# Performance work log

Measured on AMD Instinct MI355X. Metric: run time of the kernel, lower is better.

## Reference

```python
import jax, jax.numpy as jnp
import numpy as np

EPS = 1e-7
BETA = 1.0


def setup_inputs() -> dict:
    key = jax.random.key(0)
    k1, k2, k3, k4 = jax.random.split(key, 4)
    N, E, D_IN, D_OUT = 50000, 800000, 96, 96
    feat = jax.random.normal(k1, (N, D_IN), dtype=jnp.float32)
    src = jax.random.randint(k2, (E,), 0, N, dtype=jnp.int32)
    dst = jax.random.randint(k3, (E,), 0, N, dtype=jnp.int32)
    W = jax.random.normal(k4, (D_IN, D_OUT), dtype=jnp.float32) / np.sqrt(D_IN)
    b = jnp.zeros((D_OUT,), dtype=jnp.float32)
    return {"feat": feat, "src": src, "dst": dst, "W": W, "b": b}


def reference(feat, src, dst, W, b):
    # GENConv with softmax aggregation (canonical DeeperGCN semantics):
    # per edge e=(u,v): m_e = relu(h_u) + eps
    #                   a_e = softmax over edges into v of (beta * m_e)  (per feature dim)
    #                   msg_v = sum_e a_e * m_e
    # out = MLP(h + msg), MLP here = single Linear (mlp_layers=1)
    N = feat.shape[0]
    m = jax.nn.relu(feat[src]) + EPS                     # [E, D]
    logits = BETA * m                                    # [E, D]
    # numerically stable segment softmax over incoming edges of each dst node
    seg_max = jax.ops.segment_max(logits, dst, num_segments=N)   # [N, D]
    ex = jnp.exp(logits - seg_max[dst])                  # [E, D]
    denom = jax.ops.segment_sum(ex, dst, num_segments=N)         # [N, D]
    a = ex / denom[dst]                                  # [E, D]
    msg = jax.ops.segment_sum(a * m, dst, num_segments=N)        # [N, D]
    feats = feat + msg                                   # residual
    return feats @ W + b                                 # [N, D_out]
```

## Files before the change

### kernel.cpp

```cpp
#include <hip/hip_runtime.h>

#define D 96
#define EPSV 1e-7f
#define STRIDE 64
#define NB 16
#define TFUSED 192
#define EPB 2048
#define CAP 5120
#define HLP 100

__device__ __forceinline__ unsigned short f32_to_bf16_rtne(float x) {
    unsigned int u = __float_as_uint(x);
    u += 0x7fffu + ((u >> 16) & 1u);
    return (unsigned short)(u >> 16);
}
__device__ __forceinline__ float blo(uint u) { return __uint_as_float(u << 16); }
__device__ __forceinline__ float bhi(uint u) { return __uint_as_float(u & 0xFFFF0000u); }

__device__ __forceinline__ ushort4 conv_m4(const float4 f) {
    ushort4 o;
    o.x = f32_to_bf16_rtne(fmaxf(f.x, 0.f) + EPSV);
    o.y = f32_to_bf16_rtne(fmaxf(f.y, 0.f) + EPSV);
    o.z = f32_to_bf16_rtne(fmaxf(f.z, 0.f) + EPSV);
    o.w = f32_to_bf16_rtne(fmaxf(f.w, 0.f) + EPSV);
    return o;
}

__global__ __launch_bounds__(256) void part_conv(
    const int* __restrict__ src, const int* __restrict__ dst,
    uint* __restrict__ cursor,
    uint* __restrict__ stage,
    int E, int pblk,
    const float* __restrict__ feat, ushort* __restrict__ fb, int total4)
{
    __shared__ uint   hist[256];
    __shared__ uint   scn[256];
    __shared__ uint   xbase[256];
    __shared__ uint   gbase[256];
    __shared__ uint   sorted[EPB];
    __shared__ ushort sbid[EPB];

    int t = threadIdx.x;

    if ((int)blockIdx.x >= pblk) {
        int i = ((int)blockIdx.x - pblk) * 256 + t;
        if (i < total4)
            reinterpret_cast<ushort4*>(fb)[i] =
                conv_m4(reinterpret_cast<const float4*>(feat)[i]);
        return;
    }

    int e0 = blockIdx.x * EPB;
    int tot = E - e0; if (tot > EPB) tot = EPB;

    hist[t] = 0;
    __syncthreads();

    uint myb[EPB / 256], myrk[EPB / 256], myrec[EPB / 256];
    #pragma unroll
    for (int r = 0; r < EPB / 256; ++r) {
        int i = r * 256 + t;
        if (i < tot) {
            int d = dst[e0 + i];
            int s = src[e0 + i];
            uint b = (uint)d >> 8;
            myb[r]  = b;
            myrk[r] = atomicAdd(&hist[b], 1u);
            myrec[r] = (uint)(s & 0xFFFF) | ((uint)(d & 0xFF) << 16);
        }
    }
    __syncthreads();

    scn[t] = hist[t];
    __syncthreads();
    #pragma unroll
    for (int off = 1; off < 256; off <<= 1) {
        uint v = (t >= off) ? scn[t - off] : 0u;
        __syncthreads();
        scn[t] += v;
        __syncthreads();
    }
    xbase[t] = scn[t] - hist[t];
    if (hist[t] > 0)
        gbase[t] = (uint)t * CAP + atomicAdd(&cursor[t], hist[t]);
    __syncthreads();

    #pragma unroll
    for (int r = 0; r < EPB / 256; ++r) {
        int i = r * 256 + t;
        if (i < tot) {
            uint j = xbase[myb[r]] + myrk[r];
            sorted[j] = myrec[r];
            sbid[j]   = (ushort)myb[r];
        }
    }
    __syncthreads();

    #pragma unroll
    for (int r = 0; r < EPB / 256; ++r) {
        int j = r * 256 + t;
        if (j < tot) {
            uint b = sbid[j];
            uint gaddr = gbase[b] + ((uint)j - xbase[b]);
            if (gaddr - b * CAP < CAP)
                stage[gaddr] = sorted[j];
        }
    }
}

__global__ __launch_bounds__(256) void csr_build(
    const uint* __restrict__ cursor, const uint* __restrict__ stage,
    int* __restrict__ deg, ushort* __restrict__ csr, int N)
{
    __shared__ int ldeg[256];
    int b = blockIdx.x;
    int t = threadIdx.x;
    ldeg[t] = 0;
    __syncthreads();

    int cnt = (int)cursor[b]; if (cnt > CAP) cnt = CAP;
    const uint* sp = stage + (size_t)b * CAP;
    for (int i = t; i < cnt; i += 256) {
        uint rec = sp[i];
        int s  = rec & 0xFFFF;
        int dl = (rec >> 16) & 0xFF;
        int slot = atomicAdd(&ldeg[dl], 1);
        if (slot < STRIDE)
            csr[(size_t)((b << 8) + dl) * STRIDE + slot] = (ushort)s;
    }
    __syncthreads();
    int n = (b << 8) + t;
    if (n < N) deg[n] = min(ldeg[t], STRIDE);
}

__global__ __launch_bounds__(256) void build_fast(
    const float* __restrict__ feat, ushort* __restrict__ fb, int total4,
    const int* __restrict__ src, const int* __restrict__ dst,
    int* __restrict__ deg, ushort* __restrict__ csr, int E)
{
    int i = blockIdx.x * 256 + threadIdx.x;
    if (i < total4) {
        reinterpret_cast<ushort4*>(fb)[i] =
            conv_m4(reinterpret_cast<const float4*>(feat)[i]);
    } else {
        int e = i - total4;
        if (e < E) {
            int d = dst[e];
            int pos = atomicAdd(&deg[d], 1);
            if (pos < STRIDE) csr[(size_t)d * STRIDE + pos] = (ushort)src[e];
        }
    }
}

__global__ __launch_bounds__(TFUSED, 4) void fused_gather_gemm(
    const float* __restrict__ feat,
    const ushort* __restrict__ fb,
    const int* __restrict__ degp,
    const ushort* __restrict__ csr,
    const float* __restrict__ W,
    const float* __restrict__ bias,
    float* __restrict__ out,
    int N)
{
    __shared__ float  hl[NB][HLP];
    __shared__ ushort csr_l[NB * STRIDE];
    __shared__ int    degl[NB];

    int t = threadIdx.x;
    int nb0 = blockIdx.x * NB;

    {
        int nodes = N - nb0; if (nodes > NB) nodes = NB;
        int avail4 = (nodes * STRIDE) / 8;
        const uint4* gsrc = reinterpret_cast<const uint4*>(csr + (size_t)nb0 * STRIDE);
        uint4* ldst = reinterpret_cast<uint4*>(csr_l);
        if (t < avail4) ldst[t] = gsrc[t];
        if (t >= 128 && t < 128 + NB) {
            int nl = t - 128;
            int n = nb0 + nl;
            degl[nl] = (n < N) ? min(degp[n], STRIDE) : 0;
        }
    }
    __syncthreads();

    {
        int nl = t / 12;
        int q  = (t % 12) * 8;
        int n  = nb0 + nl;
        if (n < N) {
            int c = degl[nl];
            const ushort* cl = &csr_l[nl * STRIDE];

            float d0=0.f,d1=0.f,d2=0.f,d3=0.f,d4=0.f,d5=0.f,d6=0.f,d7=0.f;
            float a0=0.f,a1=0.f,a2=0.f,a3=0.f,a4=0.f,a5=0.f,a6=0.f,a7=0.f;

            #define PROC8(U) { \
                float m0 = blo((U).x), m1 = bhi((U).x); \
                float m2 = blo((U).y), m3 = bhi((U).y); \
                float m4 = blo((U).z), m5 = bhi((U).z); \
                float m6 = blo((U).w), m7 = bhi((U).w); \
                float e0=__expf(m0), e1=__expf(m1), e2=__expf(m2), e3=__expf(m3); \
                float e4=__expf(m4), e5=__expf(m5), e6=__expf(m6), e7=__expf(m7); \
                d0+=e0; d1+=e1; d2+=e2; d3+=e3; d4+=e4; d5+=e5; d6+=e6; d7+=e7; \
                a0=fmaf(e0,m0,a0); a1=fmaf(e1,m1,a1); a2=fmaf(e2,m2,a2); a3=fmaf(e3,m3,a3); \
                a4=fmaf(e4,m4,a4); a5=fmaf(e5,m5,a5); a6=fmaf(e6,m6,a6); a7=fmaf(e7,m7,a7); }

            int j = 0;
            for (; j + 4 <= c; j += 4) {
                const ushort4 ia = *reinterpret_cast<const ushort4*>(cl + j);
                const uint4 u0 = *reinterpret_cast<const uint4*>(fb + (size_t)ia.x * D + q);
                const uint4 u1 = *reinterpret_cast<const uint4*>(fb + (size_t)ia.y * D + q);
                const uint4 u2 = *reinterpret_cast<const uint4*>(fb + (size_t)ia.z * D + q);
                const uint4 u3 = *reinterpret_cast<const uint4*>(fb + (size_t)ia.w * D + q);
                PROC8(u0); PROC8(u1); PROC8(u2); PROC8(u3);
            }
            for (; j < c; ++j) {
                int s = cl[j];
                const uint4 u = *reinterpret_cast<const uint4*>(fb + (size_t)s * D + q);
                PROC8(u);
            }
            #undef PROC8

            const float4 bA = *reinterpret_cast<const float4*>(feat + (size_t)n * D + q);
            const float4 bB = *reinterpret_cast<const float4*>(feat + (size_t)n * D + q + 4);
            bool has = c > 0;
            float4 hA, hB;
            hA.x = bA.x + (has ? a0 / d0 : 0.f);
            hA.y = bA.y + (has ? a1 / d1 : 0.f);
            hA.z = bA.z + (has ? a2 / d2 : 0.f);
            hA.w = bA.w + (has ? a3 / d3 : 0.f);
            hB.x = bB.x + (has ? a4 / d4 : 0.f);
            hB.y = bB.y + (has ? a5 / d5 : 0.f);
            hB.z = bB.z + (has ? a6 / d6 : 0.f);
            hB.w = bB.w + (has ? a7 / d7 : 0.f);
            *reinterpret_cast<float4*>(&hl[nl][q])     = hA;
            *reinterpret_cast<float4*>(&hl[nl][q + 4]) = hB;
        }
    }
    __syncthreads();

    int q   = (t % 24) * 4;
    int grp = t / 24;
    int r0 = grp * 2, r1 = r0 + 1;
    float4 acc0 = *reinterpret_cast<const float4*>(bias + q);
    float4 acc1 = acc0;

    #pragma unroll 4
    for (int k = 0; k < D; ++k) {
        const float4 w = *reinterpret_cast<const float4*>(W + k * D + q);
        float h0 = hl[r0][k];
        float h1 = hl[r1][k];
        acc0.x = fmaf(h0, w.x, acc0.x); acc0.y = fmaf(h0, w.y, acc0.y);
        acc0.z = fmaf(h0, w.z, acc0.z); acc0.w = fmaf(h0, w.w, acc0.w);
        acc1.x = fmaf(h1, w.x, acc1.x); acc1.y = fmaf(h1, w.y, acc1.y);
        acc1.z = fmaf(h1, w.z, acc1.z); acc1.w = fmaf(h1, w.w, acc1.w);
    }

    int n0 = nb0 + r0;
    if (n0 + 0 < N) *reinterpret_cast<float4*>(out + (size_t)(n0 + 0) * D + q) = acc0;
    if (n0 + 1 < N) *reinterpret_cast<float4*>(out + (size_t)(n0 + 1) * D + q) = acc1;
}

extern "C" void kernel_launch(void* const* d_in, const int* in_sizes, int n_in,
                              void* d_out, int out_size, void* d_ws, size_t ws_size,
                              hipStream_t stream) {
    const float* feat = (const float*)d_in[0];
    const int*   src  = (const int*)d_in[1];
    const int*   dst  = (const int*)d_in[2];
    const float* W    = (const float*)d_in[3];
    const float* bias = (const float*)d_in[4];

    int N = in_sizes[0] / D;
    int E = in_sizes[1];
    int total4 = N * D / 4;
    int nbuck  = (N + 255) >> 8;

    size_t fb_bytes    = (size_t)N * D * sizeof(ushort);
    size_t deg_bytes   = (size_t)N * sizeof(int);
    size_t csr_bytes   = (size_t)N * STRIDE * sizeof(ushort);
    size_t cur_bytes   = 256 * sizeof(uint);
    size_t stage_bytes = (size_t)nbuck * CAP * sizeof(uint);

    size_t part_need  = fb_bytes + deg_bytes + csr_bytes + cur_bytes + stage_bytes;
    size_t fast_need  = fb_bytes + deg_bytes + csr_bytes;

    int gblocks = (N + NB - 1) / NB;

    ushort* fb  = (ushort*)d_ws;
    int*    deg = (int*)((char*)d_ws + fb_bytes);
    ushort* csr = (ushort*)((char*)deg + deg_bytes);

    if (ws_size >= part_need) {
        uint* cursor = (uint*)((char*)csr + csr_bytes);
        uint* stage  = (uint*)((char*)cursor + cur_bytes);

        int pblk = (E + EPB - 1) / EPB;
        int cblk = (total4 + 255) / 256;

        (void)hipMemsetAsync(cursor, 0, cur_bytes, stream);
        part_conv<<<pblk + cblk, 256, 0, stream>>>(
            src, dst, cursor, stage, E, pblk, feat, fb, total4);
        csr_build<<<nbuck, 256, 0, stream>>>(cursor, stage, deg, csr, N);
        fused_gather_gemm<<<gblocks, TFUSED, 0, stream>>>(
            feat, fb, deg, csr, W, bias, (float*)d_out, N);
    } else if (ws_size >= fast_need) {
        (void)hipMemsetAsync(deg, 0, deg_bytes, stream);
        int btotal = total4 + E;
        build_fast<<<(btotal + 255) / 256, 256, 0, stream>>>(
            feat, fb, total4, src, dst, deg, csr, E);
        fused_gather_gemm<<<gblocks, TFUSED, 0, stream>>>(
            feat, fb, deg, csr, W, bias, (float*)d_out, N);
    }
}
```

Before: 82.98 us.

## Sort nodes by degree within buckets and use exp2 with prescaled features

csr_build now emits a per-bucket permutation of nodes grouped by clamped in-degree. The fused gather/GEMM kernel processes nodes in that order, so threads in a wavefront have similar loop trip counts, reducing divergence and tail imbalance. Features are also pre-multiplied by log2(e) at bf16 conversion so the inner loop can use exp2f, with the aggregated result rescaled by ln2. This adds an indirection through perm, scattered output rows, and extra bf16 rounding of scaled values.

Result: slower. 98.27 us (+18.4%).

```diff
diff --git a/kernel.cpp b/kernel.cpp
--- a/kernel.cpp
+++ b/kernel.cpp
@@ -8,6 +8,8 @@
 #define EPB 2048
 #define CAP 5120
 #define HLP 100
+#define LOG2E 1.4426950408889634f
+#define LN2   0.6931471805599453f
 
 __device__ __forceinline__ unsigned short f32_to_bf16_rtne(float x) {
     unsigned int u = __float_as_uint(x);
@@ -19,10 +21,10 @@
 
 __device__ __forceinline__ ushort4 conv_m4(const float4 f) {
     ushort4 o;
-    o.x = f32_to_bf16_rtne(fmaxf(f.x, 0.f) + EPSV);
-    o.y = f32_to_bf16_rtne(fmaxf(f.y, 0.f) + EPSV);
-    o.z = f32_to_bf16_rtne(fmaxf(f.z, 0.f) + EPSV);
-    o.w = f32_to_bf16_rtne(fmaxf(f.w, 0.f) + EPSV);
+    o.x = f32_to_bf16_rtne((fmaxf(f.x, 0.f) + EPSV) * LOG2E);
+    o.y = f32_to_bf16_rtne((fmaxf(f.y, 0.f) + EPSV) * LOG2E);
+    o.z = f32_to_bf16_rtne((fmaxf(f.z, 0.f) + EPSV) * LOG2E);
+    o.w = f32_to_bf16_rtne((fmaxf(f.w, 0.f) + EPSV) * LOG2E);
     return o;
 }
 
@@ -110,12 +112,17 @@
 
 __global__ __launch_bounds__(256) void csr_build(
     const uint* __restrict__ cursor, const uint* __restrict__ stage,
-    int* __restrict__ deg, ushort* __restrict__ csr, int N)
+    int* __restrict__ deg, ushort* __restrict__ csr, int* __restrict__ perm,
+    int N)
 {
     __shared__ int ldeg[256];
+    __shared__ int bins[STRIDE + 1];
+    __shared__ int binbase[STRIDE + 1];
+
     int b = blockIdx.x;
     int t = threadIdx.x;
     ldeg[t] = 0;
+    if (t <= STRIDE) bins[t] = 0;
     __syncthreads();
 
     int cnt = (int)cursor[b]; if (cnt > CAP) cnt = CAP;
@@ -129,8 +136,24 @@
             csr[(size_t)((b << 8) + dl) * STRIDE + slot] = (ushort)s;
     }
     __syncthreads();
-    int n = (b << 8) + t;
-    if (n < N) deg[n] = min(ldeg[t], STRIDE);
+
+    int nodes = N - (b << 8); if (nodes > 256) nodes = 256;
+    int dcl = 0;
+    if (t < nodes) {
+        dcl = min(ldeg[t], STRIDE);
+        deg[(b << 8) + t] = dcl;
+        atomicAdd(&bins[dcl], 1);
+    }
+    __syncthreads();
+    if (t == 0) {
+        int run = 0;
+        for (int i = 0; i <= STRIDE; ++i) { binbase[i] = run; run += bins[i]; bins[i] = 0; }
+    }
+    __syncthreads();
+    if (t < nodes) {
+        int r = atomicAdd(&bins[dcl], 1);
+        perm[(b << 8) + binbase[dcl] + r] = (b << 8) + t;
+    }
 }
 
 __global__ __launch_bounds__(256) void build_fast(
@@ -152,11 +175,13 @@
     }
 }
 
+template<bool PERM>
 __global__ __launch_bounds__(TFUSED, 4) void fused_gather_gemm(
     const float* __restrict__ feat,
     const ushort* __restrict__ fb,
     const int* __restrict__ degp,
     const ushort* __restrict__ csr,
+    const int* __restrict__ perm,
     const float* __restrict__ W,
     const float* __restrict__ bias,
     float* __restrict__ out,
@@ -164,30 +189,35 @@
 {
     __shared__ float  hl[NB][HLP];
     __shared__ ushort csr_l[NB * STRIDE];
+    __shared__ int    pl[NB];
     __shared__ int    degl[NB];
 
     int t = threadIdx.x;
     int nb0 = blockIdx.x * NB;
 
-    {
-        int nodes = N - nb0; if (nodes > NB) nodes = NB;
-        int avail4 = (nodes * STRIDE) / 8;
-        const uint4* gsrc = reinterpret_cast<const uint4*>(csr + (size_t)nb0 * STRIDE);
-        uint4* ldst = reinterpret_cast<uint4*>(csr_l);
-        if (t < avail4) ldst[t] = gsrc[t];
-        if (t >= 128 && t < 128 + NB) {
-            int nl = t - 128;
-            int n = nb0 + nl;
-            degl[nl] = (n < N) ? min(degp[n], STRIDE) : 0;
-        }
+    if (t < NB) {
+        int idx = nb0 + t;
+        int n = -1;
+        if (idx < N) n = PERM ? perm[idx] : idx;
+        pl[t] = n;
+        degl[t] = (n >= 0) ? min(degp[n], STRIDE) : 0;
+    }
+    __syncthreads();
+
+    if (t < NB * 8) {
+        int nl = t >> 3, w = t & 7;
+        int n = pl[nl];
+        if (n >= 0)
+            reinterpret_cast<uint4*>(csr_l)[t] =
+                reinterpret_cast<const uint4*>(csr + (size_t)n * STRIDE)[w];
     }
     __syncthreads();
 
     {
         int nl = t / 12;
         int q  = (t % 12) * 8;
-        int n  = nb0 + nl;
-        if (n < N) {
+        int n  = pl[nl];
+        if (n >= 0) {
             int c = degl[nl];
             const ushort* cl = &csr_l[nl * STRIDE];
 
@@ -199,8 +229,8 @@
                 float m2 = blo((U).y), m3 = bhi((U).y); \
                 float m4 = blo((U).z), m5 = bhi((U).z); \
                 float m6 = blo((U).w), m7 = bhi((U).w); \
-                float e0=__expf(m0), e1=__expf(m1), e2=__expf(m2), e3=__expf(m3); \
-                float e4=__expf(m4), e5=__expf(m5), e6=__expf(m6), e7=__expf(m7); \
+                float e0=exp2f(m0), e1=exp2f(m1), e2=exp2f(m2), e3=exp2f(m3); \
+                float e4=exp2f(m4), e5=exp2f(m5), e6=exp2f(m6), e7=exp2f(m7); \
                 d0+=e0; d1+=e1; d2+=e2; d3+=e3; d4+=e4; d5+=e5; d6+=e6; d7+=e7; \
                 a0=fmaf(e0,m0,a0); a1=fmaf(e1,m1,a1); a2=fmaf(e2,m2,a2); a3=fmaf(e3,m3,a3); \
                 a4=fmaf(e4,m4,a4); a5=fmaf(e5,m5,a5); a6=fmaf(e6,m6,a6); a7=fmaf(e7,m7,a7); }
@@ -225,14 +255,14 @@
             const float4 bB = *reinterpret_cast<const float4*>(feat + (size_t)n * D + q + 4);
             bool has = c > 0;
             float4 hA, hB;
-            hA.x = bA.x + (has ? a0 / d0 : 0.f);
-            hA.y = bA.y + (has ? a1 / d1 : 0.f);
-            hA.z = bA.z + (has ? a2 / d2 : 0.f);
-            hA.w = bA.w + (has ? a3 / d3 : 0.f);
-            hB.x = bB.x + (has ? a4 / d4 : 0.f);
-            hB.y = bB.y + (has ? a5 / d5 : 0.f);
-            hB.z = bB.z + (has ? a6 / d6 : 0.f);
-            hB.w = bB.w + (has ? a7 / d7 : 0.f);
+            hA.x = bA.x + (has ? LN2 * (a0 / d0) : 0.f);
+            hA.y = bA.y + (has ? LN2 * (a1 / d1) : 0.f);
+            hA.z = bA.z + (has ? LN2 * (a2 / d2) : 0.f);
+            hA.w = bA.w + (has ? LN2 * (a3 / d3) : 0.f);
+            hB.x = bB.x + (has ? LN2 * (a4 / d4) : 0.f);
+            hB.y = bB.y + (has ? LN2 * (a5 / d5) : 0.f);
+            hB.z = bB.z + (has ? LN2 * (a6 / d6) : 0.f);
+            hB.w = bB.w + (has ? LN2 * (a7 / d7) : 0.f);
             *reinterpret_cast<float4*>(&hl[nl][q])     = hA;
             *reinterpret_cast<float4*>(&hl[nl][q + 4]) = hB;
         }
@@ -256,9 +286,9 @@
         acc1.z = fmaf(h1, w.z, acc1.z); acc1.w = fmaf(h1, w.w, acc1.w);
     }
 
-    int n0 = nb0 + r0;
-    if (n0 + 0 < N) *reinterpret_cast<float4*>(out + (size_t)(n0 + 0) * D + q) = acc0;
-    if (n0 + 1 < N) *reinterpret_cast<float4*>(out + (size_t)(n0 + 1) * D + q) = acc1;
+    int na = pl[r0], nb = pl[r1];
+    if (na >= 0) *reinterpret_cast<float4*>(out + (size_t)na * D + q) = acc0;
+    if (nb >= 0) *reinterpret_cast<float4*>(out + (size_t)nb * D + q) = acc1;
 }
 
 extern "C" void kernel_launch(void* const* d_in, const int* in_sizes, int n_in,
@@ -277,22 +307,23 @@
 
     size_t fb_bytes    = (size_t)N * D * sizeof(ushort);
     size_t deg_bytes   = (size_t)N * sizeof(int);
+    size_t perm_bytes  = (size_t)N * sizeof(int);
     size_t csr_bytes   = (size_t)N * STRIDE * sizeof(ushort);
     size_t cur_bytes   = 256 * sizeof(uint);
     size_t stage_bytes = (size_t)nbuck * CAP * sizeof(uint);
 
-    size_t part_need  = fb_bytes + deg_bytes + csr_bytes + cur_bytes + stage_bytes;
-    size_t fast_need  = fb_bytes + deg_bytes + csr_bytes;
+    size_t part_need = fb_bytes + deg_bytes + perm_bytes + csr_bytes + cur_bytes + stage_bytes;
+    size_t fast_need = fb_bytes + deg_bytes + csr_bytes;
 
     int gblocks = (N + NB - 1) / NB;
 
-    ushort* fb  = (ushort*)d_ws;
-    int*    deg = (int*)((char*)d_ws + fb_bytes);
-    ushort* csr = (ushort*)((char*)deg + deg_bytes);
-
     if (ws_size >= part_need) {
-        uint* cursor = (uint*)((char*)csr + csr_bytes);
-        uint* stage  = (uint*)((char*)cursor + cur_bytes);
+        ushort* fb     = (ushort*)d_ws;
+        int*    deg    = (int*)((char*)d_ws + fb_bytes);
+        int*    perm   = (int*)((char*)deg + deg_bytes);
+        ushort* csr    = (ushort*)((char*)perm + perm_bytes);
+        uint*   cursor = (uint*)((char*)csr + csr_bytes);
+        uint*   stage  = (uint*)((char*)cursor + cur_bytes);
 
         int pblk = (E + EPB - 1) / EPB;
         int cblk = (total4 + 255) / 256;
@@ -300,15 +331,19 @@
         (void)hipMemsetAsync(cursor, 0, cur_bytes, stream);
         part_conv<<<pblk + cblk, 256, 0, stream>>>(
             src, dst, cursor, stage, E, pblk, feat, fb, total4);
-        csr_build<<<nbuck, 256, 0, stream>>>(cursor, stage, deg, csr, N);
-        fused_gather_gemm<<<gblocks, TFUSED, 0, stream>>>(
-            feat, fb, deg, csr, W, bias, (float*)d_out, N);
+        csr_build<<<nbuck, 256, 0, stream>>>(cursor, stage, deg, csr, perm, N);
+        fused_gather_gemm<true><<<gblocks, TFUSED, 0, stream>>>(
+            feat, fb, deg, csr, perm, W, bias, (float*)d_out, N);
     } else if (ws_size >= fast_need) {
+        ushort* fb  = (ushort*)d_ws;
+        int*    deg = (int*)((char*)d_ws + fb_bytes);
+        ushort* csr = (ushort*)((char*)deg + deg_bytes);
+
         (void)hipMemsetAsync(deg, 0, deg_bytes, stream);
         int btotal = total4 + E;
         build_fast<<<(btotal + 255) / 256, 256, 0, stream>>>(
             feat, fb, total4, src, dst, deg, csr, E);
-        fused_gather_gemm<<<gblocks, TFUSED, 0, stream>>>(
-            feat, fb, deg, csr, W, bias, (float*)d_out, N);
-    }
-}
+        fused_gather_gemm<false><<<gblocks, TFUSED, 0, stream>>>(
+            feat, fb, deg, csr, nullptr, W, bias, (float*)d_out, N);
+    }
+}
```
